# Performance work log

Hardware: AMD Instinct MI355X
Metric: run time of the kernel (lower is better)

## Reference

```python
import jax, jax.numpy as jnp
import numpy as np

N, L, D, H = 16384, 50, 64, 1
N_ITEMS, N_CATS, N_RATINGS = 100000, 1000, 5


def setup_inputs() -> dict:
    key = jax.random.key(0)
    ks = jax.random.split(key, 16)
    s = 1.0 / np.sqrt(D)
    return {
        "nodes": jax.random.randint(ks[0], (N,), 0, N_ITEMS),
        "history_vc": jax.random.randint(ks[1], (N, L), 0, N_CATS),
        "history_r": jax.random.randint(ks[2], (N, L), 0, N_RATINGS),
        "c2e": jax.random.normal(ks[3], (N_CATS, D), jnp.float32),
        "v2e": jax.random.normal(ks[4], (N_ITEMS, D), jnp.float32),
        "r2e": jax.random.normal(ks[5], (N_RATINGS, D), jnp.float32),
        "W1": jax.random.normal(ks[6], (2 * D, D), jnp.float32) * s,
        "b1": jnp.zeros((D,), jnp.float32),
        "Wq": jax.random.normal(ks[7], (D, D), jnp.float32) * s,
        "bq": jnp.zeros((D,), jnp.float32),
        "Wk": jax.random.normal(ks[8], (D, D), jnp.float32) * s,
        "bk": jnp.zeros((D,), jnp.float32),
        "Wv": jax.random.normal(ks[9], (D, D), jnp.float32) * s,
        "bv": jnp.zeros((D,), jnp.float32),
        "Wo": jax.random.normal(ks[10], (D, D), jnp.float32) * s,
        "bo": jnp.zeros((D,), jnp.float32),
    }


def reference(nodes, history_vc, history_r, c2e, v2e, r2e,
              W1, b1, Wq, bq, Wk, bk, Wv, bv, Wo, bo):
    dh = D // H
    # ragged gather+concat, batched: vc=True -> categories for history, item rep for node
    e_vc = c2e[history_vc]                       # [N, L, D]
    e_r = r2e[history_r]                         # [N, L, D]
    x = jnp.concatenate([e_vc, e_r], axis=-1)    # [N, L, 2D]
    h = jax.nn.relu(jnp.einsum('nle,ed->nld', x, W1) + b1)  # [N, L, D]
    vc_rep = v2e[nodes]                          # [N, D]
    # cross-attention: single query per node over its history
    q = (vc_rep @ Wq + bq).reshape(N, H, dh)                      # [N, H, dh]
    k = (jnp.einsum('nld,de->nle', h, Wk) + bk).reshape(N, L, H, dh)
    v = (jnp.einsum('nld,de->nle', h, Wv) + bv).reshape(N, L, H, dh)
    scores = jnp.einsum('nhd,nlhd->nhl', q, k) / jnp.sqrt(jnp.float32(dh))
    attn = jax.nn.softmax(scores, axis=-1)                        # [N, H, L]
    ctx = jnp.einsum('nhl,nlhd->nhd', attn, v).reshape(N, D)      # [N, D]
    return ctx @ Wo + bo                                          # [N, D]
```

## Files before the change

### kernel.cpp

```cpp
#include <hip/hip_runtime.h>
#include <hip/hip_bf16.h>

#define LL 50
#define DD 64
#define NCATS 1000
#define NRAT 5

#define OFF_H    0
#define OFF_M1T  640000
#define OFF_WVOT 648192
#define OFF_BKQ  656384
#define OFF_BVO  656640

typedef __attribute__((ext_vector_type(8))) short short8;
typedef __attribute__((ext_vector_type(4))) float f32x4;

union U4S8 { uint4 u4; short8 s8; };

__device__ __forceinline__ float rlanef(float v, int l) {
  return __uint_as_float(__builtin_amdgcn_readlane(__float_as_uint(v), l));
}
__device__ __forceinline__ unsigned short f2bf(float f) {
  unsigned int u = __float_as_uint(f);
  u = (u + 0x7fffu + ((u >> 16) & 1u)) >> 16;
  return (unsigned short)u;
}
__device__ __forceinline__ unsigned int pk2bf(float lo, float hi) {
  return (unsigned int)f2bf(lo) | ((unsigned int)f2bf(hi) << 16);
}
__device__ __forceinline__ short8 pack8(float4 f0, float4 f1) {
  U4S8 t;
  t.u4.x = pk2bf(f0.x, f0.y); t.u4.y = pk2bf(f0.z, f0.w);
  t.u4.z = pk2bf(f1.x, f1.y); t.u4.w = pk2bf(f1.z, f1.w);
  return t.s8;
}

__global__ __launch_bounds__(256) void prep_fast(
    const float* __restrict__ c2e, const float* __restrict__ r2e,
    const float* __restrict__ W1, const float* __restrict__ b1,
    const float* __restrict__ Wq, const float* __restrict__ bq,
    const float* __restrict__ Wk, const float* __restrict__ Wv,
    const float* __restrict__ Wo, const float* __restrict__ bv,
    const float* __restrict__ bo, char* __restrict__ ws) {
  unsigned short* H = (unsigned short*)(ws + OFF_H);
  unsigned short* M1T = (unsigned short*)(ws + OFF_M1T);
  unsigned short* WVOT = (unsigned short*)(ws + OFF_WVOT);
  float* BKQ = (float*)(ws + OFF_BKQ);
  float* BVO = (float*)(ws + OFF_BVO);

  __shared__ float AcS[16][68];
  __shared__ float ArS[5][68];

  const int tid = threadIdx.x;
  const int wid = tid >> 6;
  const int lane = tid & 63;
  const int kg = lane >> 4;
  const int rw = lane & 15;
  const int b = blockIdx.x;

  if (b < 63) {
    const int crow = min(b * 16 + rw, NCATS - 1);
    const float* __restrict__ xc = c2e + (size_t)crow * DD;
    const float* __restrict__ xr = r2e + (size_t)min(rw, NRAT - 1) * DD;
    short8 ac_[2], ar_[2], bfa[2], bfb[2];
#pragma unroll
    for (int ks = 0; ks < 2; ++ks) {
      const int k0 = ks * 32 + kg * 8;
      ac_[ks] = pack8(*(const float4*)(xc + k0), *(const float4*)(xc + k0 + 4));
      ar_[ks] = pack8(*(const float4*)(xr + k0), *(const float4*)(xr + k0 + 4));
      U4S8 ta, tb;
#pragma unroll
      for (int j = 0; j < 4; ++j) {
        const int k = k0 + 2 * j;
        const int col = wid * 16 + rw;
        ((unsigned int*)&ta)[j] = pk2bf(W1[(size_t)k * DD + col],
                                        W1[(size_t)(k + 1) * DD + col]);
        ((unsigned int*)&tb)[j] = pk2bf(W1[(size_t)(DD + k) * DD + col],
                                        W1[(size_t)(DD + k + 1) * DD + col]);
      }
      bfa[ks] = ta.s8;
      bfb[ks] = tb.s8;
    }
    f32x4 accc = {0.f, 0.f, 0.f, 0.f}, accr = {0.f, 0.f, 0.f, 0.f};
#pragma unroll
    for (int ks = 0; ks < 2; ++ks) {
      accc = __builtin_amdgcn_mfma_f32_16x16x32_bf16(ac_[ks], bfa[ks], accc, 0, 0, 0);
      accr = __builtin_amdgcn_mfma_f32_16x16x32_bf16(ar_[ks], bfb[ks], accr, 0, 0, 0);
    }
#pragma unroll
    for (int r = 0; r < 4; ++r) {
      const int m = kg * 4 + r;
      AcS[m][wid * 16 + rw] = accc[r];
      if (m < NRAT) ArS[m][wid * 16 + rw] = accr[r];
    }
    __syncthreads();

    const float b1v = b1[lane];
    float ar5[NRAT];
#pragma unroll
    for (int r = 0; r < NRAT; ++r) ar5[r] = ArS[r][lane] + b1v;
#pragma unroll
    for (int i = 0; i < 4; ++i) {
      const int vc = b * 16 + wid * 4 + i;
      if (vc < NCATS) {
        const float acv = AcS[wid * 4 + i][lane];
#pragma unroll
        for (int r = 0; r < NRAT; ++r) {
          H[((size_t)vc * NRAT + r) * DD + lane] = f2bf(fmaxf(acv + ar5[r], 0.f));
        }
      }
    }
  } else if (b == 63) {
    short8 aq[2];
#pragma unroll
    for (int ks = 0; ks < 2; ++ks) {
      const float* __restrict__ p = Wq + (size_t)(wid * 16 + rw) * DD + ks * 32 + kg * 8;
      aq[ks] = pack8(*(const float4*)(p), *(const float4*)(p + 4));
    }
#pragma unroll
    for (int n0 = 0; n0 < 4; ++n0) {
      f32x4 a = {0.f, 0.f, 0.f, 0.f};
#pragma unroll
      for (int ks = 0; ks < 2; ++ks) {
        const float* __restrict__ p = Wk + (size_t)(n0 * 16 + rw) * DD + ks * 32 + kg * 8;
        const short8 bf = pack8(*(const float4*)(p), *(const float4*)(p + 4));
        a = __builtin_amdgcn_mfma_f32_16x16x32_bf16(aq[ks], bf, a, 0, 0, 0);
      }
#pragma unroll
      for (int r = 0; r < 4; ++r) {
        M1T[(size_t)(n0 * 16 + rw) * DD + wid * 16 + kg * 4 + r] = f2bf(a[r]);
      }
    }
    if (wid == 0) {
      const float* __restrict__ wrow = Wk + (size_t)lane * DD;
      float a0 = 0.f, a1 = 0.f, a2 = 0.f, a3 = 0.f;
#pragma unroll
      for (int t = 0; t < DD; t += 4) {
        const float4 w4 = *(const float4*)(wrow + t);
        a0 = fmaf(w4.x, bq[t + 0], a0);
        a1 = fmaf(w4.y, bq[t + 1], a1);
        a2 = fmaf(w4.z, bq[t + 2], a2);
        a3 = fmaf(w4.w, bq[t + 3], a3);
      }
      BKQ[lane] = (a0 + a1) + (a2 + a3);
    }
  } else {
    short8 ao[2];
#pragma unroll
    for (int ks = 0; ks < 2; ++ks) {
      U4S8 t4;
#pragma unroll
      for (int j = 0; j < 4; ++j) {
        const int k = ks * 32 + kg * 8 + 2 * j;
        const int col = wid * 16 + rw;
        ((unsigned int*)&t4)[j] = pk2bf(Wo[(size_t)k * DD + col],
                                        Wo[(size_t)(k + 1) * DD + col]);
      }
      ao[ks] = t4.s8;
    }
#pragma unroll
    for (int n0 = 0; n0 < 4; ++n0) {
      f32x4 a = {0.f, 0.f, 0.f, 0.f};
#pragma unroll
      for (int ks = 0; ks < 2; ++ks) {
        const float* __restrict__ p = Wv + (size_t)(n0 * 16 + rw) * DD + ks * 32 + kg * 8;
        const short8 bf = pack8(*(const float4*)(p), *(const float4*)(p + 4));
        a = __builtin_amdgcn_mfma_f32_16x16x32_bf16(ao[ks], bf, a, 0, 0, 0);
      }
#pragma unroll
      for (int r = 0; r < 4; ++r) {
        WVOT[(size_t)(wid * 16 + kg * 4 + r) * DD + n0 * 16 + rw] = f2bf(a[r]);
      }
    }
    if (wid == 0) {
      float acc = bo[lane];
#pragma unroll 8
      for (int t = 0; t < DD; ++t) acc = fmaf(bv[t], Wo[(size_t)t * DD + lane], acc);
      BVO[lane] = acc;
    }
  }
}

__global__ __launch_bounds__(256, 5) void vc_main(
    const int* __restrict__ nodes, const int* __restrict__ hvc,
    const int* __restrict__ hr, const float* __restrict__ v2e,
    const char* __restrict__ ws, float* __restrict__ out, int N) {
  const unsigned short* __restrict__ H = (const unsigned short*)(ws + OFF_H);
  const unsigned short* __restrict__ M1T = (const unsigned short*)(ws + OFF_M1T);
  const unsigned short* __restrict__ WVOT = (const unsigned short*)(ws + OFF_WVOT);
  const float* __restrict__ BKQ = (const float*)(ws + OFF_BKQ);
  const float* __restrict__ BVO = (const float*)(ws + OFF_BVO);

  __shared__ __align__(16) char smem[25600 + 1088 + 1088];
  char* HlB = smem;
  float* gS = (float*)(smem + 25600);
  float* ctxS = (float*)(smem + 25600 + 1088);

  const int tid = threadIdx.x;
  const int wid = tid >> 6;
  const int lane = tid & 63;
  const int kg = lane >> 4;
  const int rw = lane & 15;
  const int nb = blockIdx.x * 4;
  const int n = min(nb + wid, N - 1);

  const int lidx = (lane < LL) ? lane : 0;
  const int idx = hvc[(size_t)n * LL + lidx] * NRAT + hr[(size_t)n * LL + lidx];

  {
    const int chunk = lane & 7;
    char* wbase = HlB + wid * 6400;
#pragma unroll
    for (int i = 0; i < 7; ++i) {
      const int s = (i < 6) ? (i * 8 + (lane >> 3)) : (42 + (lane >> 3));
      const int sidx = __shfl(idx, s, 64);
      const char* src = (const char*)H + (size_t)sidx * 128 + ((chunk ^ (s & 7)) << 4);
      __builtin_amdgcn_global_load_lds(
          (const __attribute__((address_space(1))) void*)src,
          (__attribute__((address_space(3))) void*)(wbase + ((i < 6) ? i * 1024 : 5376)),
          16, 0, 0);
    }
  }

  {
    const int node_id = nodes[min(nb + (rw & 3), N - 1)];
    const float* __restrict__ xrow = v2e + (size_t)node_id * DD;
    short8 xa[2];
#pragma unroll
    for (int ks = 0; ks < 2; ++ks) {
      const float4 f0 = *(const float4*)(xrow + ks * 32 + kg * 8);
      const float4 f1 = *(const float4*)(xrow + ks * 32 + kg * 8 + 4);
      U4S8 t;
      t.u4.x = pk2bf(f0.x, f0.y); t.u4.y = pk2bf(f0.z, f0.w);
      t.u4.z = pk2bf(f1.x, f1.y); t.u4.w = pk2bf(f1.z, f1.w);
      xa[ks] = t.s8;
    }
    const int n0 = wid;
    f32x4 a = {0.f, 0.f, 0.f, 0.f};
#pragma unroll
    for (int ks = 0; ks < 2; ++ks) {
      const short8 bf = *(const short8*)(M1T + (n0 * 16 + rw) * DD + ks * 32 + kg * 8);
      a = __builtin_amdgcn_mfma_f32_16x16x32_bf16(xa[ks], bf, a, 0, 0, 0);
    }
    if (kg == 0) {
      const float bkqv = BKQ[n0 * 16 + rw];
#pragma unroll
      for (int r = 0; r < 4; ++r) gS[r * 68 + n0 * 16 + rw] = a[r] + bkqv;
    }
  }
  __syncthreads();
  asm volatile("s_waitcnt vmcnt(0)" ::: "memory");
  __builtin_amdgcn_sched_barrier(0);

  const unsigned short* __restrict__ wH = (const unsigned short*)(HlB + wid * 6400);

  short8 ga[2];
#pragma unroll
  for (int ks = 0; ks < 2; ++ks) {
    const float* __restrict__ gp = gS + wid * 68 + ks * 32 + kg * 8;
    const float4 f0 = *(const float4*)(gp);
    const float4 f1 = *(const float4*)(gp + 4);
    U4S8 t;
    t.u4.x = pk2bf(f0.x, f0.y); t.u4.y = pk2bf(f0.z, f0.w);
    t.u4.z = pk2bf(f1.x, f1.y); t.u4.w = pk2bf(f1.z, f1.w);
    ga[ks] = t.s8;
  }
  float s0, s1, s2, s3;
  {
    f32x4 a;
#pragma unroll
    for (int lt = 0; lt < 4; ++lt) {
      const int s = lt * 16 + rw;
      a = (f32x4){0.f, 0.f, 0.f, 0.f};
#pragma unroll
      for (int ks = 0; ks < 2; ++ks) {
        const int c = (ks * 4 + kg) ^ (s & 7);
        U4S8 hb;
        hb.u4 = *(const uint4*)(wH + s * 64 + c * 8);
        a = __builtin_amdgcn_mfma_f32_16x16x32_bf16(ga[ks], hb.s8, a, 0, 0, 0);
      }
      if (lt == 0) s0 = a[0];
      else if (lt == 1) s1 = a[0];
      else if (lt == 2) s2 = a[0];
      else s3 = a[0];
    }
  }
  s0 *= 0.125f; s1 *= 0.125f; s2 *= 0.125f;
  s3 = (rw < 2) ? s3 * 0.125f : -INFINITY;

  float m = fmaxf(fmaxf(s0, s1), fmaxf(s2, s3));
#pragma unroll
  for (int x = 1; x <= 8; x <<= 1) m = fmaxf(m, __shfl_xor(m, x, 64));
  float e0 = __expf(s0 - m), e1 = __expf(s1 - m), e2 = __expf(s2 - m);
  float e3 = (rw < 2) ? __expf(s3 - m) : 0.f;
  float Z = ((e0 + e1) + (e2 + e3));
#pragma unroll
  for (int x = 1; x <= 8; x <<= 1) Z += __shfl_xor(Z, x, 64);
  const float invZ = 1.f / Z;

  {
    const int sub = (lane & 7) * 2;
    const int hi3 = lane >> 3;
    float c0 = 0.f, c1 = 0.f;
#define CTX_BLOCK(EREG, BASE, CNT, CACC)                                        \
    _Pragma("unroll")                                                           \
    for (int j = 0; j < (CNT); ++j) {                                           \
      const int l = (BASE) + j;                                                 \
      const unsigned short hbb = *(const unsigned short*)(                      \
          (const char*)wH + l * 128 + (((hi3 ^ (l & 7)) << 4) | sub));          \
      CACC = fmaf(__uint_as_float(((unsigned int)hbb) << 16),                   \
                  rlanef(EREG, j), CACC);                                       \
    }
    CTX_BLOCK(e0, 0, 16, c0)
    CTX_BLOCK(e1, 16, 16, c1)
    CTX_BLOCK(e2, 32, 16, c0)
    CTX_BLOCK(e3, 48, 2, c1)
#undef CTX_BLOCK
    ctxS[wid * 68 + lane] = (c0 + c1) * invZ;
  }
  __syncthreads();

  {
    short8 ca[2];
#pragma unroll
    for (int ks = 0; ks < 2; ++ks) {
      const float* __restrict__ cp = ctxS + (rw & 3) * 68 + ks * 32 + kg * 8;
      const float4 f0 = *(const float4*)(cp);
      const float4 f1 = *(const float4*)(cp + 4);
      U4S8 t;
      t.u4.x = pk2bf(f0.x, f0.y); t.u4.y = pk2bf(f0.z, f0.w);
      t.u4.z = pk2bf(f1.x, f1.y); t.u4.w = pk2bf(f1.z, f1.w);
      ca[ks] = t.s8;
    }
    const int n0 = wid;
    f32x4 a = {0.f, 0.f, 0.f, 0.f};
#pragma unroll
    for (int ks = 0; ks < 2; ++ks) {
      const short8 bf = *(const short8*)(WVOT + (n0 * 16 + rw) * DD + ks * 32 + kg * 8);
      a = __builtin_amdgcn_mfma_f32_16x16x32_bf16(ca[ks], bf, a, 0, 0, 0);
    }
    if (kg == 0) {
      const float bvov = BVO[n0 * 16 + rw];
#pragma unroll
      for (int r = 0; r < 4; ++r) {
        const int node = nb + r;
        if (node < N) out[(size_t)node * DD + n0 * 16 + rw] = a[r] + bvov;
      }
    }
  }
}

extern "C" void kernel_launch(void* const* d_in, const int* in_sizes, int n_in,
                              void* d_out, int out_size, void* d_ws, size_t ws_size,
                              hipStream_t stream) {
  const int* nodes = (const int*)d_in[0];
  const int* hvc = (const int*)d_in[1];
  const int* hr = (const int*)d_in[2];
  const float* c2e = (const float*)d_in[3];
  const float* v2e = (const float*)d_in[4];
  const float* r2e = (const float*)d_in[5];
  const float* W1 = (const float*)d_in[6];
  const float* b1 = (const float*)d_in[7];
  const float* Wq = (const float*)d_in[8];
  const float* bq = (const float*)d_in[9];
  const float* Wk = (const float*)d_in[10];
  const float* bk = (const float*)d_in[11];
  const float* Wv = (const float*)d_in[12];
  const float* bv = (const float*)d_in[13];
  const float* Wo = (const float*)d_in[14];
  const float* bo = (const float*)d_in[15];
  (void)bk;
  float* out = (float*)d_out;
  char* ws = (char*)d_ws;

  const int N = in_sizes[0];

  prep_fast<<<65, 256, 0, stream>>>(c2e, r2e, W1, b1, Wq, bq, Wk, Wv, Wo, bv, bo, ws);
  vc_main<<<(N + 3) / 4, 256, 0, stream>>>(nodes, hvc, hr, v2e, ws, out, N);
}
```

Before: 36.57 us.

## Process two nodes per wave with direct global H reads and prefetching

Each wave now handles two nodes sequentially instead of four waves cooperating on four nodes. The LDS staging of the gathered H rows through global_load_lds is dropped. The score MFMAs and the context accumulation now read the 5000-row H table straight from global memory, relying on L2/L1 since the table is small. Index and query-embedding loads for the second node are prefetched during the first. Block-wide barriers go away, at the cost of a 4x-redundant MFMA per wave (only row 0 used) and more global load latency on the critical path.

```diff
diff --git a/kernel.cpp b/kernel.cpp
--- a/kernel.cpp
+++ b/kernel.cpp
@@ -181,7 +181,7 @@
   }
 }
 
-__global__ __launch_bounds__(256, 5) void vc_main(
+__global__ __launch_bounds__(256) void vc_main(
     const int* __restrict__ nodes, const int* __restrict__ hvc,
     const int* __restrict__ hr, const float* __restrict__ v2e,
     const char* __restrict__ ws, float* __restrict__ out, int N) {
@@ -191,162 +191,151 @@
   const float* __restrict__ BKQ = (const float*)(ws + OFF_BKQ);
   const float* __restrict__ BVO = (const float*)(ws + OFF_BVO);
 
-  __shared__ __align__(16) char smem[25600 + 1088 + 1088];
-  char* HlB = smem;
-  float* gS = (float*)(smem + 25600);
-  float* ctxS = (float*)(smem + 25600 + 1088);
+  __shared__ float gS[4][68];
+  __shared__ float ctxS[4][68];
 
   const int tid = threadIdx.x;
   const int wid = tid >> 6;
   const int lane = tid & 63;
   const int kg = lane >> 4;
   const int rw = lane & 15;
-  const int nb = blockIdx.x * 4;
-  const int n = min(nb + wid, N - 1);
-
   const int lidx = (lane < LL) ? lane : 0;
-  const int idx = hvc[(size_t)n * LL + lidx] * NRAT + hr[(size_t)n * LL + lidx];
-
+
+  const int nwave = blockIdx.x * 4 + wid;
+
+  const int nA = min(nwave * 2, N - 1);
+  int idx_cur = hvc[(size_t)nA * LL + lidx] * NRAT + hr[(size_t)nA * LL + lidx];
+  int nid_cur = nodes[nA];
+  float4 xf_cur[4];
   {
-    const int chunk = lane & 7;
-    char* wbase = HlB + wid * 6400;
-#pragma unroll
-    for (int i = 0; i < 7; ++i) {
-      const int s = (i < 6) ? (i * 8 + (lane >> 3)) : (42 + (lane >> 3));
-      const int sidx = __shfl(idx, s, 64);
-      const char* src = (const char*)H + (size_t)sidx * 128 + ((chunk ^ (s & 7)) << 4);
-      __builtin_amdgcn_global_load_lds(
-          (const __attribute__((address_space(1))) void*)src,
-          (__attribute__((address_space(3))) void*)(wbase + ((i < 6) ? i * 1024 : 5376)),
-          16, 0, 0);
+    const float* __restrict__ xrow = v2e + (size_t)nid_cur * DD;
+#pragma unroll
+    for (int ks = 0; ks < 2; ++ks) {
+      xf_cur[2 * ks + 0] = *(const float4*)(xrow + ks * 32 + kg * 8);
+      xf_cur[2 * ks + 1] = *(const float4*)(xrow + ks * 32 + kg * 8 + 4);
     }
   }
 
-  {
-    const int node_id = nodes[min(nb + (rw & 3), N - 1)];
-    const float* __restrict__ xrow = v2e + (size_t)node_id * DD;
-    short8 xa[2];
-#pragma unroll
-    for (int ks = 0; ks < 2; ++ks) {
-      const float4 f0 = *(const float4*)(xrow + ks * 32 + kg * 8);
-      const float4 f1 = *(const float4*)(xrow + ks * 32 + kg * 8 + 4);
-      U4S8 t;
-      t.u4.x = pk2bf(f0.x, f0.y); t.u4.y = pk2bf(f0.z, f0.w);
-      t.u4.z = pk2bf(f1.x, f1.y); t.u4.w = pk2bf(f1.z, f1.w);
-      xa[ks] = t.s8;
-    }
-    const int n0 = wid;
-    f32x4 a = {0.f, 0.f, 0.f, 0.f};
-#pragma unroll
-    for (int ks = 0; ks < 2; ++ks) {
-      const short8 bf = *(const short8*)(M1T + (n0 * 16 + rw) * DD + ks * 32 + kg * 8);
-      a = __builtin_amdgcn_mfma_f32_16x16x32_bf16(xa[ks], bf, a, 0, 0, 0);
-    }
-    if (kg == 0) {
-      const float bkqv = BKQ[n0 * 16 + rw];
-#pragma unroll
-      for (int r = 0; r < 4; ++r) gS[r * 68 + n0 * 16 + rw] = a[r] + bkqv;
-    }
-  }
-  __syncthreads();
-  asm volatile("s_waitcnt vmcnt(0)" ::: "memory");
-  __builtin_amdgcn_sched_barrier(0);
-
-  const unsigned short* __restrict__ wH = (const unsigned short*)(HlB + wid * 6400);
-
-  short8 ga[2];
-#pragma unroll
-  for (int ks = 0; ks < 2; ++ks) {
-    const float* __restrict__ gp = gS + wid * 68 + ks * 32 + kg * 8;
-    const float4 f0 = *(const float4*)(gp);
-    const float4 f1 = *(const float4*)(gp + 4);
-    U4S8 t;
-    t.u4.x = pk2bf(f0.x, f0.y); t.u4.y = pk2bf(f0.z, f0.w);
-    t.u4.z = pk2bf(f1.x, f1.y); t.u4.w = pk2bf(f1.z, f1.w);
-    ga[ks] = t.s8;
-  }
-  float s0, s1, s2, s3;
-  {
-    f32x4 a;
-#pragma unroll
-    for (int lt = 0; lt < 4; ++lt) {
-      const int s = lt * 16 + rw;
-      a = (f32x4){0.f, 0.f, 0.f, 0.f};
+  int idx_nxt = 0, nid_nxt = 0;
+  float4 xf_nxt[4];
+
+#pragma unroll
+  for (int g = 0; g < 2; ++g) {
+    const int n = min(nwave * 2 + g, N - 1);
+
+    if (g == 0) {
+      const int nB = min(nwave * 2 + 1, N - 1);
+      idx_nxt = hvc[(size_t)nB * LL + lidx] * NRAT + hr[(size_t)nB * LL + lidx];
+      nid_nxt = nodes[nB];
+      const float* __restrict__ xrow = v2e + (size_t)nid_nxt * DD;
 #pragma unroll
       for (int ks = 0; ks < 2; ++ks) {
-        const int c = (ks * 4 + kg) ^ (s & 7);
-        U4S8 hb;
-        hb.u4 = *(const uint4*)(wH + s * 64 + c * 8);
-        a = __builtin_amdgcn_mfma_f32_16x16x32_bf16(ga[ks], hb.s8, a, 0, 0, 0);
-      }
-      if (lt == 0) s0 = a[0];
-      else if (lt == 1) s1 = a[0];
-      else if (lt == 2) s2 = a[0];
-      else s3 = a[0];
-    }
-  }
-  s0 *= 0.125f; s1 *= 0.125f; s2 *= 0.125f;
-  s3 = (rw < 2) ? s3 * 0.125f : -INFINITY;
-
-  float m = fmaxf(fmaxf(s0, s1), fmaxf(s2, s3));
-#pragma unroll
-  for (int x = 1; x <= 8; x <<= 1) m = fmaxf(m, __shfl_xor(m, x, 64));
-  float e0 = __expf(s0 - m), e1 = __expf(s1 - m), e2 = __expf(s2 - m);
-  float e3 = (rw < 2) ? __expf(s3 - m) : 0.f;
-  float Z = ((e0 + e1) + (e2 + e3));
-#pragma unroll
-  for (int x = 1; x <= 8; x <<= 1) Z += __shfl_xor(Z, x, 64);
-  const float invZ = 1.f / Z;
-
-  {
-    const int sub = (lane & 7) * 2;
-    const int hi3 = lane >> 3;
-    float c0 = 0.f, c1 = 0.f;
-#define CTX_BLOCK(EREG, BASE, CNT, CACC)                                        \
-    _Pragma("unroll")                                                           \
-    for (int j = 0; j < (CNT); ++j) {                                           \
-      const int l = (BASE) + j;                                                 \
-      const unsigned short hbb = *(const unsigned short*)(                      \
-          (const char*)wH + l * 128 + (((hi3 ^ (l & 7)) << 4) | sub));          \
-      CACC = fmaf(__uint_as_float(((unsigned int)hbb) << 16),                   \
-                  rlanef(EREG, j), CACC);                                       \
-    }
-    CTX_BLOCK(e0, 0, 16, c0)
-    CTX_BLOCK(e1, 16, 16, c1)
-    CTX_BLOCK(e2, 32, 16, c0)
-    CTX_BLOCK(e3, 48, 2, c1)
+        xf_nxt[2 * ks + 0] = *(const float4*)(xrow + ks * 32 + kg * 8);
+        xf_nxt[2 * ks + 1] = *(const float4*)(xrow + ks * 32 + kg * 8 + 4);
+      }
+    }
+    const int idx = idx_cur;
+
+    {
+      short8 xa[2];
+      xa[0] = pack8(xf_cur[0], xf_cur[1]);
+      xa[1] = pack8(xf_cur[2], xf_cur[3]);
+#pragma unroll
+      for (int n0 = 0; n0 < 4; ++n0) {
+        f32x4 a = {0.f, 0.f, 0.f, 0.f};
+#pragma unroll
+        for (int ks = 0; ks < 2; ++ks) {
+          const short8 bf = *(const short8*)(M1T + (size_t)(n0 * 16 + rw) * DD + ks * 32 + kg * 8);
+          a = __builtin_amdgcn_mfma_f32_16x16x32_bf16(xa[ks], bf, a, 0, 0, 0);
+        }
+        if (kg == 0) gS[wid][n0 * 16 + rw] = a[0] + BKQ[n0 * 16 + rw];
+      }
+    }
+    short8 ga[2];
+#pragma unroll
+    for (int ks = 0; ks < 2; ++ks) {
+      const float* __restrict__ gp = &gS[wid][ks * 32 + kg * 8];
+      ga[ks] = pack8(*(const float4*)(gp), *(const float4*)(gp + 4));
+    }
+
+    int bidx[4];
+#pragma unroll
+    for (int lt = 0; lt < 4; ++lt) bidx[lt] = __shfl(idx, lt * 16 + rw, 64);
+    float s0, s1, s2, s3;
+    {
+      f32x4 a;
+#pragma unroll
+      for (int lt = 0; lt < 4; ++lt) {
+        a = (f32x4){0.f, 0.f, 0.f, 0.f};
+#pragma unroll
+        for (int ks = 0; ks < 2; ++ks) {
+          U4S8 hb;
+          hb.u4 = *(const uint4*)(H + (size_t)bidx[lt] * DD + ks * 32 + kg * 8);
+          a = __builtin_amdgcn_mfma_f32_16x16x32_bf16(ga[ks], hb.s8, a, 0, 0, 0);
+        }
+        if (lt == 0) s0 = a[0];
+        else if (lt == 1) s1 = a[0];
+        else if (lt == 2) s2 = a[0];
+        else s3 = a[0];
+      }
+    }
+    s0 *= 0.125f; s1 *= 0.125f; s2 *= 0.125f;
+    s3 = (rw < 2) ? s3 * 0.125f : -INFINITY;
+
+    float m = fmaxf(fmaxf(s0, s1), fmaxf(s2, s3));
+#pragma unroll
+    for (int x = 1; x <= 8; x <<= 1) m = fmaxf(m, __shfl_xor(m, x, 64));
+    float e0 = __expf(s0 - m), e1 = __expf(s1 - m), e2 = __expf(s2 - m);
+    float e3 = (rw < 2) ? __expf(s3 - m) : 0.f;
+    float Z = ((e0 + e1) + (e2 + e3));
+#pragma unroll
+    for (int x = 1; x <= 8; x <<= 1) Z += __shfl_xor(Z, x, 64);
+    const float invZ = 1.f / Z;
+
+    {
+      float c0 = 0.f, c1 = 0.f;
+#define CTX_BLOCK(EREG, BASE, CNT, CACC)                                   \
+      _Pragma("unroll")                                                    \
+      for (int j = 0; j < (CNT); ++j) {                                    \
+        const int l = (BASE) + j;                                          \
+        const int si = __builtin_amdgcn_readlane(idx, l);                  \
+        const unsigned short hbb = H[(size_t)si * DD + lane];              \
+        CACC = fmaf(__uint_as_float(((unsigned int)hbb) << 16),            \
+                    rlanef(EREG, j), CACC);                                \
+      }
+      CTX_BLOCK(e0, 0, 16, c0)
+      CTX_BLOCK(e1, 16, 16, c1)
+      CTX_BLOCK(e2, 32, 16, c0)
+      CTX_BLOCK(e3, 48, 2, c1)
 #undef CTX_BLOCK
-    ctxS[wid * 68 + lane] = (c0 + c1) * invZ;
-  }
-  __syncthreads();
-
-  {
-    short8 ca[2];
-#pragma unroll
-    for (int ks = 0; ks < 2; ++ks) {
-      const float* __restrict__ cp = ctxS + (rw & 3) * 68 + ks * 32 + kg * 8;
-      const float4 f0 = *(const float4*)(cp);
-      const float4 f1 = *(const float4*)(cp + 4);
-      U4S8 t;
-      t.u4.x = pk2bf(f0.x, f0.y); t.u4.y = pk2bf(f0.z, f0.w);
-      t.u4.z = pk2bf(f1.x, f1.y); t.u4.w = pk2bf(f1.z, f1.w);
-      ca[ks] = t.s8;
-    }
-    const int n0 = wid;
-    f32x4 a = {0.f, 0.f, 0.f, 0.f};
-#pragma unroll
-    for (int ks = 0; ks < 2; ++ks) {
-      const short8 bf = *(const short8*)(WVOT + (n0 * 16 + rw) * DD + ks * 32 + kg * 8);
-      a = __builtin_amdgcn_mfma_f32_16x16x32_bf16(ca[ks], bf, a, 0, 0, 0);
-    }
-    if (kg == 0) {
-      const float bvov = BVO[n0 * 16 + rw];
-#pragma unroll
-      for (int r = 0; r < 4; ++r) {
-        const int node = nb + r;
-        if (node < N) out[(size_t)node * DD + n0 * 16 + rw] = a[r] + bvov;
-      }
-    }
+      ctxS[wid][lane] = (c0 + c1) * invZ;
+    }
+
+    {
+      short8 ca[2];
+#pragma unroll
+      for (int ks = 0; ks < 2; ++ks) {
+        const float* __restrict__ cp = &ctxS[wid][ks * 32 + kg * 8];
+        ca[ks] = pack8(*(const float4*)(cp), *(const float4*)(cp + 4));
+      }
+#pragma unroll
+      for (int n0 = 0; n0 < 4; ++n0) {
+        f32x4 a = {0.f, 0.f, 0.f, 0.f};
+#pragma unroll
+        for (int ks = 0; ks < 2; ++ks) {
+          const short8 bf = *(const short8*)(WVOT + (size_t)(n0 * 16 + rw) * DD + ks * 32 + kg * 8);
+          a = __builtin_amdgcn_mfma_f32_16x16x32_bf16(ca[ks], bf, a, 0, 0, 0);
+        }
+        if (kg == 0 && n < N) {
+          out[(size_t)n * DD + n0 * 16 + rw] = a[0] + BVO[n0 * 16 + rw];
+        }
+      }
+    }
+
+    idx_cur = idx_nxt;
+    nid_cur = nid_nxt;
+#pragma unroll
+    for (int i = 0; i < 4; ++i) xf_cur[i] = xf_nxt[i];
   }
 }
 
@@ -376,5 +365,5 @@
   const int N = in_sizes[0];
 
   prep_fast<<<65, 256, 0, stream>>>(c2e, r2e, W1, b1, Wq, bq, Wk, Wv, Wo, bv, bo, ws);
-  vc_main<<<(N + 3) / 4, 256, 0, stream>>>(nodes, hvc, hr, v2e, ws, out, N);
-}
+  vc_main<<<(N + 7) / 8, 256, 0, stream>>>(nodes, hvc, hr, v2e, ws, out, N);
+}
```

Result: slower. 60.84 us (+66.4%).

## Split prep table build per rating across more blocks and use hardware bf16 pack

Applied to the files above, without the earlier changes.

The prep kernel's category-times-rating table build is spread over 315 blocks (one per category tile and rating) instead of 63. Each block now computes its rating projection with scalar FMAs instead of a second MFMA. The software round-to-nearest bf16 conversion is replaced by the v_cvt_pk_bf16_f32 instruction in both kernels. The goal is to shorten the prep kernel's critical path through more parallelism and to cut conversion ALU work in the main kernel. The cost is redundant W1 and c2e loads across the five rating blocks.

```diff
diff --git a/kernel.cpp b/kernel.cpp
--- a/kernel.cpp
+++ b/kernel.cpp
@@ -20,13 +20,15 @@
 __device__ __forceinline__ float rlanef(float v, int l) {
   return __uint_as_float(__builtin_amdgcn_readlane(__float_as_uint(v), l));
 }
+__device__ __forceinline__ unsigned int pk2bf(float lo, float hi) {
+  unsigned int r;
+  asm("v_cvt_pk_bf16_f32 %0, %1, %2" : "=v"(r) : "v"(lo), "v"(hi));
+  return r;
+}
 __device__ __forceinline__ unsigned short f2bf(float f) {
-  unsigned int u = __float_as_uint(f);
-  u = (u + 0x7fffu + ((u >> 16) & 1u)) >> 16;
-  return (unsigned short)u;
-}
-__device__ __forceinline__ unsigned int pk2bf(float lo, float hi) {
-  return (unsigned int)f2bf(lo) | ((unsigned int)f2bf(hi) << 16);
+  unsigned int r;
+  asm("v_cvt_pk_bf16_f32 %0, %1, %1" : "=v"(r) : "v"(f));
+  return (unsigned short)r;
 }
 __device__ __forceinline__ short8 pack8(float4 f0, float4 f1) {
   U4S8 t;
@@ -49,7 +51,6 @@
   float* BVO = (float*)(ws + OFF_BVO);
 
   __shared__ float AcS[16][68];
-  __shared__ float ArS[5][68];
 
   const int tid = threadIdx.x;
   const int wid = tid >> 6;
@@ -58,59 +59,51 @@
   const int rw = lane & 15;
   const int b = blockIdx.x;
 
-  if (b < 63) {
-    const int crow = min(b * 16 + rw, NCATS - 1);
+  if (b < 315) {
+    const int t = b / 5;
+    const int r = b - t * 5;
+
+    const int crow = min(t * 16 + rw, NCATS - 1);
     const float* __restrict__ xc = c2e + (size_t)crow * DD;
-    const float* __restrict__ xr = r2e + (size_t)min(rw, NRAT - 1) * DD;
-    short8 ac_[2], ar_[2], bfa[2], bfb[2];
+    f32x4 accc = {0.f, 0.f, 0.f, 0.f};
 #pragma unroll
     for (int ks = 0; ks < 2; ++ks) {
       const int k0 = ks * 32 + kg * 8;
-      ac_[ks] = pack8(*(const float4*)(xc + k0), *(const float4*)(xc + k0 + 4));
-      ar_[ks] = pack8(*(const float4*)(xr + k0), *(const float4*)(xr + k0 + 4));
-      U4S8 ta, tb;
+      const short8 ac_ = pack8(*(const float4*)(xc + k0), *(const float4*)(xc + k0 + 4));
+      U4S8 ta;
 #pragma unroll
       for (int j = 0; j < 4; ++j) {
         const int k = k0 + 2 * j;
         const int col = wid * 16 + rw;
         ((unsigned int*)&ta)[j] = pk2bf(W1[(size_t)k * DD + col],
                                         W1[(size_t)(k + 1) * DD + col]);
-        ((unsigned int*)&tb)[j] = pk2bf(W1[(size_t)(DD + k) * DD + col],
-                                        W1[(size_t)(DD + k + 1) * DD + col]);
-      }
-      bfa[ks] = ta.s8;
-      bfb[ks] = tb.s8;
-    }
-    f32x4 accc = {0.f, 0.f, 0.f, 0.f}, accr = {0.f, 0.f, 0.f, 0.f};
-#pragma unroll
-    for (int ks = 0; ks < 2; ++ks) {
-      accc = __builtin_amdgcn_mfma_f32_16x16x32_bf16(ac_[ks], bfa[ks], accc, 0, 0, 0);
-      accr = __builtin_amdgcn_mfma_f32_16x16x32_bf16(ar_[ks], bfb[ks], accr, 0, 0, 0);
-    }
-#pragma unroll
-    for (int r = 0; r < 4; ++r) {
-      const int m = kg * 4 + r;
-      AcS[m][wid * 16 + rw] = accc[r];
-      if (m < NRAT) ArS[m][wid * 16 + rw] = accr[r];
-    }
+      }
+      accc = __builtin_amdgcn_mfma_f32_16x16x32_bf16(ac_, ta.s8, accc, 0, 0, 0);
+    }
+#pragma unroll
+    for (int rr = 0; rr < 4; ++rr) AcS[kg * 4 + rr][wid * 16 + rw] = accc[rr];
+
+    const float* __restrict__ rrow = r2e + (size_t)r * DD;
+    float a0 = b1[lane], a1 = 0.f, a2 = 0.f, a3 = 0.f;
+#pragma unroll 4
+    for (int e = 0; e < DD; e += 4) {
+      a0 = fmaf(rrow[e + 0], W1[(size_t)(DD + e + 0) * DD + lane], a0);
+      a1 = fmaf(rrow[e + 1], W1[(size_t)(DD + e + 1) * DD + lane], a1);
+      a2 = fmaf(rrow[e + 2], W1[(size_t)(DD + e + 2) * DD + lane], a2);
+      a3 = fmaf(rrow[e + 3], W1[(size_t)(DD + e + 3) * DD + lane], a3);
+    }
+    const float ar = (a0 + a1) + (a2 + a3);
     __syncthreads();
 
-    const float b1v = b1[lane];
-    float ar5[NRAT];
-#pragma unroll
-    for (int r = 0; r < NRAT; ++r) ar5[r] = ArS[r][lane] + b1v;
 #pragma unroll
     for (int i = 0; i < 4; ++i) {
-      const int vc = b * 16 + wid * 4 + i;
+      const int cat = (tid >> 6) + i * 4;
+      const int vc = t * 16 + cat;
       if (vc < NCATS) {
-        const float acv = AcS[wid * 4 + i][lane];
-#pragma unroll
-        for (int r = 0; r < NRAT; ++r) {
-          H[((size_t)vc * NRAT + r) * DD + lane] = f2bf(fmaxf(acv + ar5[r], 0.f));
-        }
-      }
-    }
-  } else if (b == 63) {
+        H[((size_t)vc * NRAT + r) * DD + lane] = f2bf(fmaxf(AcS[cat][lane] + ar, 0.f));
+      }
+    }
+  } else if (b == 315) {
     short8 aq[2];
 #pragma unroll
     for (int ks = 0; ks < 2; ++ks) {
@@ -135,12 +128,12 @@
       const float* __restrict__ wrow = Wk + (size_t)lane * DD;
       float a0 = 0.f, a1 = 0.f, a2 = 0.f, a3 = 0.f;
 #pragma unroll
-      for (int t = 0; t < DD; t += 4) {
-        const float4 w4 = *(const float4*)(wrow + t);
-        a0 = fmaf(w4.x, bq[t + 0], a0);
-        a1 = fmaf(w4.y, bq[t + 1], a1);
-        a2 = fmaf(w4.z, bq[t + 2], a2);
-        a3 = fmaf(w4.w, bq[t + 3], a3);
+      for (int t2 = 0; t2 < DD; t2 += 4) {
+        const float4 w4 = *(const float4*)(wrow + t2);
+        a0 = fmaf(w4.x, bq[t2 + 0], a0);
+        a1 = fmaf(w4.y, bq[t2 + 1], a1);
+        a2 = fmaf(w4.z, bq[t2 + 2], a2);
+        a3 = fmaf(w4.w, bq[t2 + 3], a3);
       }
       BKQ[lane] = (a0 + a1) + (a2 + a3);
     }
@@ -175,7 +168,7 @@
     if (wid == 0) {
       float acc = bo[lane];
 #pragma unroll 8
-      for (int t = 0; t < DD; ++t) acc = fmaf(bv[t], Wo[(size_t)t * DD + lane], acc);
+      for (int t2 = 0; t2 < DD; ++t2) acc = fmaf(bv[t2], Wo[(size_t)t2 * DD + lane], acc);
       BVO[lane] = acc;
     }
   }
@@ -228,12 +221,8 @@
     short8 xa[2];
 #pragma unroll
     for (int ks = 0; ks < 2; ++ks) {
-      const float4 f0 = *(const float4*)(xrow + ks * 32 + kg * 8);
-      const float4 f1 = *(const float4*)(xrow + ks * 32 + kg * 8 + 4);
-      U4S8 t;
-      t.u4.x = pk2bf(f0.x, f0.y); t.u4.y = pk2bf(f0.z, f0.w);
-      t.u4.z = pk2bf(f1.x, f1.y); t.u4.w = pk2bf(f1.z, f1.w);
-      xa[ks] = t.s8;
+      xa[ks] = pack8(*(const float4*)(xrow + ks * 32 + kg * 8),
+                     *(const float4*)(xrow + ks * 32 + kg * 8 + 4));
     }
     const int n0 = wid;
     f32x4 a = {0.f, 0.f, 0.f, 0.f};
@@ -258,12 +247,7 @@
 #pragma unroll
   for (int ks = 0; ks < 2; ++ks) {
     const float* __restrict__ gp = gS + wid * 68 + ks * 32 + kg * 8;
-    const float4 f0 = *(const float4*)(gp);
-    const float4 f1 = *(const float4*)(gp + 4);
-    U4S8 t;
-    t.u4.x = pk2bf(f0.x, f0.y); t.u4.y = pk2bf(f0.z, f0.w);
-    t.u4.z = pk2bf(f1.x, f1.y); t.u4.w = pk2bf(f1.z, f1.w);
-    ga[ks] = t.s8;
+    ga[ks] = pack8(*(const float4*)(gp), *(const float4*)(gp + 4));
   }
   float s0, s1, s2, s3;
   {
@@ -325,12 +309,7 @@
 #pragma unroll
     for (int ks = 0; ks < 2; ++ks) {
       const float* __restrict__ cp = ctxS + (rw & 3) * 68 + ks * 32 + kg * 8;
-      const float4 f0 = *(const float4*)(cp);
-      const float4 f1 = *(const float4*)(cp + 4);
-      U4S8 t;
-      t.u4.x = pk2bf(f0.x, f0.y); t.u4.y = pk2bf(f0.z, f0.w);
-      t.u4.z = pk2bf(f1.x, f1.y); t.u4.w = pk2bf(f1.z, f1.w);
-      ca[ks] = t.s8;
+      ca[ks] = pack8(*(const float4*)(cp), *(const float4*)(cp + 4));
     }
     const int n0 = wid;
     f32x4 a = {0.f, 0.f, 0.f, 0.f};
@@ -375,6 +354,6 @@
 
   const int N = in_sizes[0];
 
-  prep_fast<<<65, 256, 0, stream>>>(c2e, r2e, W1, b1, Wq, bq, Wk, Wv, Wo, bv, bo, ws);
+  prep_fast<<<317, 256, 0, stream>>>(c2e, r2e, W1, b1, Wq, bq, Wk, Wv, Wo, bv, bo, ws);
   vc_main<<<(N + 3) / 4, 256, 0, stream>>>(nodes, hvc, hr, v2e, ws, out, N);
 }
```

Result: no change. 36.09 us (-1.3%).
